# Kernel tuning notes

Hardware: AMD Instinct MI355X
Metric: run time of the kernel (lower is better)

## Reference

```python
import jax, jax.numpy as jnp
import numpy as np

jax.config.update("jax_enable_x64", True)  # original uses complex128

B = 262144
K = 16


def setup_inputs() -> dict:
    key = jax.random.key(0)
    k1, k2 = jax.random.split(key)
    x = jax.random.normal(k1, (B, K), dtype=jnp.float32)
    shuffle_vector = jax.random.uniform(k2, (K,), dtype=jnp.float32)
    return {"x": x, "shuffle_vector": shuffle_vector}


def reference(x, shuffle_vector):
    # x: (B, K) real sign pattern; shuffle_vector: (K,) learned phases
    k = x.shape[1]
    b = x.shape[0]
    R = np.sqrt(1.0 + np.sin(np.pi / k))  # fixed radius (learnable_radius=False)
    radii = jnp.where(x > 0, R, 1.0 / R).astype(jnp.complex128)
    zeros = radii * jnp.exp(1j * shuffle_vector.astype(jnp.complex128))  # (B, K)

    # Vieta's formulas via sequential monomial multiplication: prod_i (z - r_i).
    # coeffs[:, d] == (-1)^d * e_d(roots), identical to the combinatorial expansion
    # in the original, but O(K^2) instead of O(2^K).
    init = jnp.zeros((b, k + 1), dtype=jnp.complex128).at[:, 0].set(1.0)

    def step(c, r):  # c: (B, K+1), r: (B,)
        shifted = jnp.concatenate([jnp.zeros((b, 1), c.dtype), c[:, :-1]], axis=1)
        return c - r[:, None] * shifted, None

    coeffs, _ = jax.lax.scan(step, init, zeros.T)  # scan over K roots

    # normalize: x / ||x||_2 * sqrt(K+1)  (torch.norm on complex = sqrt(sum |x|^2))
    l2 = jnp.sqrt(jnp.sum(jnp.abs(coeffs) ** 2, axis=-1, keepdims=True))
    return coeffs / l2 * np.sqrt(k + 1)
```

## Files before the change

### kernel.cpp

```cpp
#include <hip/hip_runtime.h>
#include <math.h>

#define KROOTS 16
#define NC 17
#define BLK 64

template <int MODE>
__global__ __launch_bounds__(BLK) void encoder_vieta_kernel(
    const float* __restrict__ x,
    const float* __restrict__ shuffle,
    float* __restrict__ out,
    int B)
{
    __shared__ float sc[KROOTS], ss[KROOTS];
    __shared__ float so[BLK * NC];

    const int tid = threadIdx.x;
    if (tid < KROOTS) {
        float phi = shuffle[tid];
        sc[tid] = cosf(phi);
        ss[tid] = sinf(phi);
    }
    __syncthreads();

    const int b = blockIdx.x * BLK + tid;
    if (b >= B) return;

    const float R    = 1.09320186720915563f;
    const float invR = 0.91474476120342423f;

    const float4* xp = reinterpret_cast<const float4*>(x + (size_t)b * KROOTS);
    float xr[KROOTS];
    #pragma unroll
    for (int i = 0; i < 4; ++i) {
        float4 v = xp[i];
        xr[4 * i + 0] = v.x;
        xr[4 * i + 1] = v.y;
        xr[4 * i + 2] = v.z;
        xr[4 * i + 3] = v.w;
    }

    float cr[NC], ci[NC];
    cr[0] = 1.0f; ci[0] = 0.0f;
    #pragma unroll
    for (int d = 1; d < NC; ++d) { cr[d] = 0.0f; ci[d] = 0.0f; }

    #pragma unroll
    for (int j = 0; j < KROOTS; ++j) {
        const float rad = (xr[j] > 0.0f) ? R : invR;
        const float rr = rad * sc[j];
        const float ri = rad * ss[j];
        #pragma unroll
        for (int d = j + 1; d >= 1; --d) {
            const float ar = cr[d - 1], ai = ci[d - 1];
            cr[d] = fmaf(-rr, ar, fmaf( ri, ai, cr[d]));
            ci[d] = fmaf(-rr, ai, fmaf(-ri, ar, ci[d]));
        }
    }

    float sum = 0.0f;
    #pragma unroll
    for (int d = 0; d < NC; ++d)
        sum = fmaf(cr[d], cr[d], fmaf(ci[d], ci[d], sum));
    const float scale = sqrtf(17.0f) * __frsqrt_rn(sum);

    if (MODE == 0) {
        float2* op = reinterpret_cast<float2*>(out + (size_t)b * 2 * NC);
        #pragma unroll
        for (int d = 0; d < NC; ++d)
            op[d] = make_float2(cr[d] * scale, ci[d] * scale);
    } else {
        #pragma unroll
        for (int d = 0; d < NC; ++d)
            so[tid * NC + d] = cr[d] * scale;
        __syncthreads();

        const size_t blk_f4 = (size_t)blockIdx.x * (BLK * NC / 4);
        float4* og = reinterpret_cast<float4*>(out) + blk_f4;
        const float4* sg = reinterpret_cast<const float4*>(so);
        #pragma unroll
        for (int i = tid; i < BLK * NC / 4; i += BLK)
            og[i] = sg[i];
    }
}

extern "C" void kernel_launch(void* const* d_in, const int* in_sizes, int n_in,
                              void* d_out, int out_size, void* d_ws, size_t ws_size,
                              hipStream_t stream) {
    const float* x       = (const float*)d_in[0];
    const float* shuffle = (const float*)d_in[1];
    float* out = (float*)d_out;
    const int B = in_sizes[0] / KROOTS;
    const int grid = (B + BLK - 1) / BLK;
    if (out_size >= 2 * NC * B) {
        encoder_vieta_kernel<0><<<grid, BLK, 0, stream>>>(x, shuffle, out, B);
    } else {
        encoder_vieta_kernel<1><<<grid, BLK, 0, stream>>>(x, shuffle, out, B);
    }
}
```

Measured before the change: 13.15 us.

## Precompute all 2^16 sign-pattern polynomials into a table and gather per row

The radii depend only on the sign of each x entry, so there are just 65536 distinct outputs. The change builds a table of every normalized real-coefficient vector in workspace once per call, then a gather kernel turns each row's signs into a 16-bit index and copies the matching table row. This swaps per-row O(K^2) complex FMAs for a 65536-row precompute plus random table reads. It adds a second launch and needs workspace of at least the table size. The gather kernel has no bounds check on B.

New measurement: 23.57 us. +79.3%, slower.

```diff
diff --git a/kernel.cpp b/kernel.cpp
--- a/kernel.cpp
+++ b/kernel.cpp
@@ -4,6 +4,109 @@
 #define KROOTS 16
 #define NC 17
 #define BLK 64
+#define TROW 20
+#define TENT 65536
+#define TBYTES ((size_t)TENT * TROW * sizeof(float))
+
+#define RAD_P 1.09320186720915563f
+#define RAD_N 0.91474476120342423f
+
+__global__ __launch_bounds__(BLK) void build_table_kernel(
+    const float* __restrict__ shuffle,
+    float* __restrict__ table)
+{
+    __shared__ float sc[KROOTS], ss[KROOTS];
+    __shared__ float so[BLK * TROW];
+
+    const int tid = threadIdx.x;
+    if (tid < KROOTS) {
+        float phi = shuffle[tid];
+        sc[tid] = cosf(phi);
+        ss[tid] = sinf(phi);
+    }
+    __syncthreads();
+
+    const unsigned idx = blockIdx.x * BLK + tid;
+
+    float cr[NC], ci[NC];
+    cr[0] = 1.0f; ci[0] = 0.0f;
+    #pragma unroll
+    for (int d = 1; d < NC; ++d) { cr[d] = 0.0f; ci[d] = 0.0f; }
+
+    #pragma unroll
+    for (int j = 0; j < KROOTS; ++j) {
+        const float rad = ((idx >> j) & 1u) ? RAD_P : RAD_N;
+        const float rr = rad * sc[j];
+        const float ri = rad * ss[j];
+        #pragma unroll
+        for (int d = j + 1; d >= 1; --d) {
+            const float ar = cr[d - 1], ai = ci[d - 1];
+            cr[d] = fmaf(-rr, ar, fmaf( ri, ai, cr[d]));
+            ci[d] = fmaf(-rr, ai, fmaf(-ri, ar, ci[d]));
+        }
+    }
+
+    float sum = 0.0f;
+    #pragma unroll
+    for (int d = 0; d < NC; ++d)
+        sum = fmaf(cr[d], cr[d], fmaf(ci[d], ci[d], sum));
+    const float scale = sqrtf(17.0f) * __frsqrt_rn(sum);
+
+    #pragma unroll
+    for (int d = 0; d < NC; ++d)
+        so[tid * TROW + d] = cr[d] * scale;
+    #pragma unroll
+    for (int d = NC; d < TROW; ++d)
+        so[tid * TROW + d] = 0.0f;
+    __syncthreads();
+
+    float4* og = reinterpret_cast<float4*>(table + (size_t)blockIdx.x * BLK * TROW);
+    const float4* sg = reinterpret_cast<const float4*>(so);
+    #pragma unroll
+    for (int i = tid; i < BLK * TROW / 4; i += BLK)
+        og[i] = sg[i];
+}
+
+__global__ __launch_bounds__(BLK) void gather_kernel(
+    const float* __restrict__ x,
+    const float* __restrict__ table,
+    float* __restrict__ out,
+    int B)
+{
+    __shared__ float so[BLK * NC];
+
+    const int tid = threadIdx.x;
+    const size_t b = (size_t)blockIdx.x * BLK + tid;
+
+    const float4* xp = reinterpret_cast<const float4*>(x + b * KROOTS);
+    unsigned idx = 0;
+    #pragma unroll
+    for (int i = 0; i < 4; ++i) {
+        float4 v = xp[i];
+        idx |= (v.x > 0.0f ? 1u : 0u) << (4 * i + 0);
+        idx |= (v.y > 0.0f ? 1u : 0u) << (4 * i + 1);
+        idx |= (v.z > 0.0f ? 1u : 0u) << (4 * i + 2);
+        idx |= (v.w > 0.0f ? 1u : 0u) << (4 * i + 3);
+    }
+
+    const float4* row = reinterpret_cast<const float4*>(table + (size_t)idx * TROW);
+    float4 r0 = row[0], r1 = row[1], r2 = row[2], r3 = row[3], r4 = row[4];
+
+    float* s = so + tid * NC;
+    s[0]=r0.x; s[1]=r0.y; s[2]=r0.z; s[3]=r0.w;
+    s[4]=r1.x; s[5]=r1.y; s[6]=r1.z; s[7]=r1.w;
+    s[8]=r2.x; s[9]=r2.y; s[10]=r2.z; s[11]=r2.w;
+    s[12]=r3.x; s[13]=r3.y; s[14]=r3.z; s[15]=r3.w;
+    s[16]=r4.x;
+    __syncthreads();
+
+    float4* og = reinterpret_cast<float4*>(out) +
+                 (size_t)blockIdx.x * (BLK * NC / 4);
+    const float4* sg = reinterpret_cast<const float4*>(so);
+    #pragma unroll
+    for (int i = tid; i < BLK * NC / 4; i += BLK)
+        og[i] = sg[i];
+}
 
 template <int MODE>
 __global__ __launch_bounds__(BLK) void encoder_vieta_kernel(
@@ -26,9 +129,6 @@
     const int b = blockIdx.x * BLK + tid;
     if (b >= B) return;
 
-    const float R    = 1.09320186720915563f;
-    const float invR = 0.91474476120342423f;
-
     const float4* xp = reinterpret_cast<const float4*>(x + (size_t)b * KROOTS);
     float xr[KROOTS];
     #pragma unroll
@@ -47,7 +147,7 @@
 
     #pragma unroll
     for (int j = 0; j < KROOTS; ++j) {
-        const float rad = (xr[j] > 0.0f) ? R : invR;
+        const float rad = (xr[j] > 0.0f) ? RAD_P : RAD_N;
         const float rr = rad * sc[j];
         const float ri = rad * ss[j];
         #pragma unroll
@@ -74,9 +174,8 @@
         for (int d = 0; d < NC; ++d)
             so[tid * NC + d] = cr[d] * scale;
         __syncthreads();
-
-        const size_t blk_f4 = (size_t)blockIdx.x * (BLK * NC / 4);
-        float4* og = reinterpret_cast<float4*>(out) + blk_f4;
+        float4* og = reinterpret_cast<float4*>(out) +
+                     (size_t)blockIdx.x * (BLK * NC / 4);
         const float4* sg = reinterpret_cast<const float4*>(so);
         #pragma unroll
         for (int i = tid; i < BLK * NC / 4; i += BLK)
@@ -92,8 +191,13 @@
     float* out = (float*)d_out;
     const int B = in_sizes[0] / KROOTS;
     const int grid = (B + BLK - 1) / BLK;
+
     if (out_size >= 2 * NC * B) {
         encoder_vieta_kernel<0><<<grid, BLK, 0, stream>>>(x, shuffle, out, B);
+    } else if (ws_size >= TBYTES) {
+        float* table = (float*)d_ws;
+        build_table_kernel<<<TENT / BLK, BLK, 0, stream>>>(shuffle, table);
+        gather_kernel<<<grid, BLK, 0, stream>>>(x, table, out, B);
     } else {
         encoder_vieta_kernel<1><<<grid, BLK, 0, stream>>>(x, shuffle, out, B);
     }
```

## Use packed FP32 FMA inline asm for complex Vieta recurrence, enlarge blocks

Applied to the files above, without the earlier changes.

Rewrites the complex multiply-accumulate recurrence with v_pk_fma_f32/v_pk_mul_f32 inline assembly, so real and imaginary parts are updated together in two packed instructions instead of four scalar FMAs. The first product for each new coefficient becomes a multiply rather than an FMA into zero, and the norm reduction is packed as well. The block size goes from 64 to 256 and the b>=B bounds check is removed, which assumes B is a multiple of the block size. The inline asm relies on op_sel and neg modifiers being correct and constrains compiler scheduling.

Measured after the change: 12.58 us. 4.3% less time.

```diff
diff --git a/kernel.cpp b/kernel.cpp
--- a/kernel.cpp
+++ b/kernel.cpp
@@ -3,33 +3,51 @@
 
 #define KROOTS 16
 #define NC 17
-#define BLK 64
+#define BLK 256
+
+#define RAD_P 1.09320186720915563f
+#define RAD_N 0.91474476120342423f
+
+typedef float v2f __attribute__((ext_vector_type(2)));
+
+__device__ __forceinline__ void cfma_neg(v2f& c, v2f rv, v2f iv, v2f p) {
+    asm("v_pk_fma_f32 %0, %1, %2, %0 neg_lo:[1,0,0] neg_hi:[1,0,0]"
+        : "+v"(c) : "v"(rv), "v"(p));
+    asm("v_pk_fma_f32 %0, %1, %2, %0 op_sel:[0,1,0] op_sel_hi:[1,0,1] neg_hi:[1,0,0]"
+        : "+v"(c) : "v"(iv), "v"(p));
+}
+
+__device__ __forceinline__ v2f cmul_neg(v2f rv, v2f iv, v2f p) {
+    v2f c;
+    asm("v_pk_mul_f32 %0, %1, %2 neg_lo:[1,0,0] neg_hi:[1,0,0]"
+        : "=v"(c) : "v"(rv), "v"(p));
+    asm("v_pk_fma_f32 %0, %1, %2, %0 op_sel:[0,1,0] op_sel_hi:[1,0,1] neg_hi:[1,0,0]"
+        : "+v"(c) : "v"(iv), "v"(p));
+    return c;
+}
 
 template <int MODE>
-__global__ __launch_bounds__(BLK) void encoder_vieta_kernel(
+__global__ __launch_bounds__(BLK) void encoder_vieta_pk(
     const float* __restrict__ x,
     const float* __restrict__ shuffle,
     float* __restrict__ out,
     int B)
 {
-    __shared__ float sc[KROOTS], ss[KROOTS];
+    __shared__ v2f scc[KROOTS], ssc[KROOTS];
     __shared__ float so[BLK * NC];
 
     const int tid = threadIdx.x;
     if (tid < KROOTS) {
         float phi = shuffle[tid];
-        sc[tid] = cosf(phi);
-        ss[tid] = sinf(phi);
+        float cv = cosf(phi), sv = sinf(phi);
+        scc[tid] = (v2f){cv, cv};
+        ssc[tid] = (v2f){sv, sv};
     }
     __syncthreads();
 
-    const int b = blockIdx.x * BLK + tid;
-    if (b >= B) return;
+    const size_t b = (size_t)blockIdx.x * BLK + tid;
 
-    const float R    = 1.09320186720915563f;
-    const float invR = 0.91474476120342423f;
-
-    const float4* xp = reinterpret_cast<const float4*>(x + (size_t)b * KROOTS);
+    const float4* xp = reinterpret_cast<const float4*>(x + b * KROOTS);
     float xr[KROOTS];
     #pragma unroll
     for (int i = 0; i < 4; ++i) {
@@ -40,43 +58,41 @@
         xr[4 * i + 3] = v.w;
     }
 
-    float cr[NC], ci[NC];
-    cr[0] = 1.0f; ci[0] = 0.0f;
-    #pragma unroll
-    for (int d = 1; d < NC; ++d) { cr[d] = 0.0f; ci[d] = 0.0f; }
+    const v2f Rv  = (v2f){RAD_P, RAD_P};
+    const v2f Iv  = (v2f){RAD_N, RAD_N};
 
+    v2f c[NC];
+    c[0] = (v2f){1.0f, 0.0f};
     #pragma unroll
     for (int j = 0; j < KROOTS; ++j) {
-        const float rad = (xr[j] > 0.0f) ? R : invR;
-        const float rr = rad * sc[j];
-        const float ri = rad * ss[j];
+        const v2f radv = (xr[j] > 0.0f) ? Rv : Iv;
+        const v2f rv = radv * scc[j];
+        const v2f iv = radv * ssc[j];
+        c[j + 1] = cmul_neg(rv, iv, c[j]);
         #pragma unroll
-        for (int d = j + 1; d >= 1; --d) {
-            const float ar = cr[d - 1], ai = ci[d - 1];
-            cr[d] = fmaf(-rr, ar, fmaf( ri, ai, cr[d]));
-            ci[d] = fmaf(-rr, ai, fmaf(-ri, ar, ci[d]));
-        }
+        for (int d = j; d >= 1; --d)
+            cfma_neg(c[d], rv, iv, c[d - 1]);
     }
 
-    float sum = 0.0f;
+    v2f s2 = c[0] * c[0];
     #pragma unroll
-    for (int d = 0; d < NC; ++d)
-        sum = fmaf(cr[d], cr[d], fmaf(ci[d], ci[d], sum));
-    const float scale = sqrtf(17.0f) * __frsqrt_rn(sum);
+    for (int d = 1; d < NC; ++d)
+        s2 = c[d] * c[d] + s2;
+    const float scale = sqrtf(17.0f) * __frsqrt_rn(s2.x + s2.y);
 
     if (MODE == 0) {
-        float2* op = reinterpret_cast<float2*>(out + (size_t)b * 2 * NC);
+        float2* op = reinterpret_cast<float2*>(out + b * 2 * NC);
         #pragma unroll
         for (int d = 0; d < NC; ++d)
-            op[d] = make_float2(cr[d] * scale, ci[d] * scale);
+            op[d] = make_float2(c[d].x * scale, c[d].y * scale);
     } else {
         #pragma unroll
         for (int d = 0; d < NC; ++d)
-            so[tid * NC + d] = cr[d] * scale;
+            so[tid * NC + d] = c[d].x * scale;
         __syncthreads();
 
-        const size_t blk_f4 = (size_t)blockIdx.x * (BLK * NC / 4);
-        float4* og = reinterpret_cast<float4*>(out) + blk_f4;
+        float4* og = reinterpret_cast<float4*>(out) +
+                     (size_t)blockIdx.x * (BLK * NC / 4);
         const float4* sg = reinterpret_cast<const float4*>(so);
         #pragma unroll
         for (int i = tid; i < BLK * NC / 4; i += BLK)
@@ -93,8 +109,8 @@
     const int B = in_sizes[0] / KROOTS;
     const int grid = (B + BLK - 1) / BLK;
     if (out_size >= 2 * NC * B) {
-        encoder_vieta_kernel<0><<<grid, BLK, 0, stream>>>(x, shuffle, out, B);
+        encoder_vieta_pk<0><<<grid, BLK, 0, stream>>>(x, shuffle, out, B);
     } else {
-        encoder_vieta_kernel<1><<<grid, BLK, 0, stream>>>(x, shuffle, out, B);
+        encoder_vieta_pk<1><<<grid, BLK, 0, stream>>>(x, shuffle, out, B);
     }
 }
```
